# Kernel optimization log

Hardware: AMD Instinct MI355X
Metric: run time of the kernel (lower is better)

Reference implementation:

```python
import jax, jax.numpy as jnp
import numpy as np

IN_FEATURES = 256
OUT_FEATURES = 256
INTERNAL = (IN_FEATURES + OUT_FEATURES) // 2  # trajectron AdditiveAttention default


def setup_inputs() -> dict:
    key = jax.random.key(0)
    k1, k2, k3, k4, k5 = jax.random.split(key, 5)
    B, TH, TQ = 32, 256, 64
    inputs = jax.random.normal(k1, (B, TH, IN_FEATURES), dtype=jnp.float32)
    state = jax.random.normal(k2, (B, TQ, OUT_FEATURES), dtype=jnp.float32)
    # Linear weights (no bias), Kaiming-ish scale
    w1 = jax.random.normal(k3, (INTERNAL, IN_FEATURES), dtype=jnp.float32) / np.sqrt(IN_FEATURES)
    w2 = jax.random.normal(k4, (INTERNAL, OUT_FEATURES), dtype=jnp.float32) / np.sqrt(OUT_FEATURES)
    v = jax.random.normal(k5, (INTERNAL,), dtype=jnp.float32) / np.sqrt(INTERNAL)
    return {"inputs": inputs, "state": state, "w1": w1, "w2": w2, "v": v, "batch_size": B}


def reference(inputs, state, w1, w2, v, batch_size):
    # history annotations: (B, Th, Din); future annotations (queries): (B, Tq, Dout)
    keys = inputs.reshape(batch_size, -1, IN_FEATURES)
    queries = state.reshape(batch_size, -1, OUT_FEATURES)
    # Additive (Bahdanau) attention: score = v . tanh(W1 k + W2 q)
    k_proj = jnp.einsum('bti,di->btd', keys, w1)       # (B, Th, D)
    q_proj = jnp.einsum('bqo,do->bqd', queries, w2)    # (B, Tq, D)
    scores = jnp.einsum('d,bqtd->bqt', v, jnp.tanh(q_proj[:, :, None, :] + k_proj[:, None, :, :]))
    alpha = jax.nn.softmax(scores, axis=-1)            # softmax over history axis
    contexts = jnp.einsum('bqt,bti->bqi', alpha, keys)  # (B, Tq, Din)
    # reshape + dropout (eval mode / p effectively 0 -> identity)
    return contexts.reshape(-1, IN_FEATURES)
```

## Files before the change

### kernel.cpp

```cpp
#include <hip/hip_runtime.h>
#include <math.h>

#define BATCH 32
#define TH    256
#define TQn   64
#define DIN   256
#define DD    256
#define QT    4
#define E2C   2.885390081777927f
#define DENMAX 1.0e9f

typedef __attribute__((ext_vector_type(8)))  short bf16x8;
typedef __attribute__((ext_vector_type(16))) float floatx16;

__device__ __forceinline__ float readlane_f(float x, int l) {
    return __int_as_float(__builtin_amdgcn_readlane(__float_as_int(x), l));
}

__device__ __forceinline__ float eclamp(float x) {
    return __builtin_amdgcn_exp2f(fminf(x * E2C, 30.f));
}

__device__ __forceinline__ void split2(float x0, float x1, unsigned& hi, unsigned& lo) {
    unsigned u0 = __float_as_uint(x0), u1 = __float_as_uint(x1);
    unsigned h0 = u0 & 0xFFFF0000u,   h1 = u1 & 0xFFFF0000u;
    float r0 = x0 - __uint_as_float(h0);
    float r1 = x1 - __uint_as_float(h1);
    hi = (u0 >> 16) | h1;
    lo = (__float_as_uint(r0) >> 16) | (__float_as_uint(r1) & 0xFFFF0000u);
}

__device__ __forceinline__ void split8(float4 f0, float4 f1, uint4& hi, uint4& lo) {
    split2(f0.x, f0.y, hi.x, lo.x);
    split2(f0.z, f0.w, hi.y, lo.y);
    split2(f1.x, f1.y, hi.z, lo.z);
    split2(f1.z, f1.w, hi.w, lo.w);
}

#define REG4  65
#define WOFF  (16 * REG4)
__global__ __launch_bounds__(256, 4)
void proj_kernel(const float* __restrict__ keys,
                 const float* __restrict__ state,
                 const float* __restrict__ w1,
                 const float* __restrict__ w2,
                 float* __restrict__ kpT,
                 float* __restrict__ qpo)
{
    __shared__ uint4 lds4[2 * 16 * REG4];

    const int bid = blockIdx.x;
    const int tid = threadIdx.x;

    const float* X;
    const float* W;
    int m0, n0;
    bool is_kp;
    if (bid < 512) {
        is_kp = true;
        m0 = (bid >> 2) * 64;
        n0 = (bid & 3) * 64;
        X = keys; W = w1;
    } else {
        is_kp = false;
        int lb = bid - 512;
        m0 = (lb >> 2) * 64;
        n0 = (lb & 3) * 64;
        X = state; W = w2;
    }

    const int w    = tid >> 6;
    const int l    = tid & 63;
    const int mt   = w >> 1;
    const int nt   = w & 1;
    const int srow = tid >> 3;
    const int kg   = tid & 7;
    const int s_s  = kg >> 1;
    const int lidx = (srow & 31) + 32 * (kg & 1);

    floatx16 acc = {};

    for (int k0 = 0; k0 < DIN; k0 += 64) {
        #pragma unroll
        for (int hrow = 0; hrow < 2; hrow++) {
            int m = srow + hrow * 32;
            const float* px = X + (size_t)(m0 + m) * DIN + k0 + kg * 8;
            uint4 hi, lo;
            split8(*(const float4*)px, *(const float4*)(px + 4), hi, lo);
            int g = m >> 5;
            lds4[((0 * 2 + g) * 4 + s_s) * REG4 + lidx] = hi;
            lds4[((2 + g) * 4 + s_s) * REG4 + lidx] = lo;
            const float* pw = W + (size_t)(n0 + m) * DIN + k0 + kg * 8;
            split8(*(const float4*)pw, *(const float4*)(pw + 4), hi, lo);
            lds4[WOFF + ((0 * 2 + g) * 4 + s_s) * REG4 + lidx] = hi;
            lds4[WOFF + ((2 + g) * 4 + s_s) * REG4 + lidx] = lo;
        }
        __syncthreads();

        #pragma unroll
        for (int s = 0; s < 4; s++) {
            uint4 ahr = lds4[((0 * 2 + mt) * 4 + s) * REG4 + l];
            uint4 alr = lds4[((2 + mt) * 4 + s) * REG4 + l];
            uint4 bhr = lds4[WOFF + ((0 * 2 + nt) * 4 + s) * REG4 + l];
            uint4 blr = lds4[WOFF + ((2 + nt) * 4 + s) * REG4 + l];
            bf16x8 ah = __builtin_bit_cast(bf16x8, ahr);
            bf16x8 al = __builtin_bit_cast(bf16x8, alr);
            bf16x8 bh = __builtin_bit_cast(bf16x8, bhr);
            bf16x8 bl = __builtin_bit_cast(bf16x8, blr);
            acc = __builtin_amdgcn_mfma_f32_32x32x16_bf16(ah, bh, acc, 0, 0, 0);
            acc = __builtin_amdgcn_mfma_f32_32x32x16_bf16(al, bh, acc, 0, 0, 0);
            acc = __builtin_amdgcn_mfma_f32_32x32x16_bf16(ah, bl, acc, 0, 0, 0);
        }
        __syncthreads();
    }

    const int col = l & 31;
    const int hl  = l >> 5;
    if (is_kp) {
        const int b  = m0 >> 8;
        const int tb = (m0 & 255) + mt * 32 + 4 * hl;
        const int d  = n0 + nt * 32 + col;
        float* p = kpT + ((size_t)b * DD + d) * TH + tb;
        #pragma unroll
        for (int g = 0; g < 4; g++)
            *(float4*)(p + 8 * g) = make_float4(eclamp(acc[4*g]),   eclamp(acc[4*g+1]),
                                                eclamp(acc[4*g+2]), eclamp(acc[4*g+3]));
    } else {
        const int d = n0 + nt * 32 + col;
        #pragma unroll
        for (int r = 0; r < 16; r++) {
            int row = (r & 3) + 8 * (r >> 2) + 4 * hl;
            qpo[(size_t)(m0 + mt * 32 + row) * DD + d] = eclamp(acc[r]);
        }
    }
}

__global__ __launch_bounds__(1024, 8)
void attn_kernel(const float* __restrict__ keys,
                 const float* __restrict__ vvec,
                 const float* __restrict__ kpT,
                 const float* __restrict__ qp,
                 float* __restrict__ out)
{
    __shared__ float s_part[4][QT][TH];
    __shared__ float s_alpha[QT][TH];
    __shared__ float s_rsum[QT];

    const int bid  = blockIdx.x;
    const int b    = bid & 31;
    const int q0   = (bid >> 5) * QT;
    const int tid  = threadIdx.x;
    const int t    = tid & 255;
    const int dgu  = __builtin_amdgcn_readfirstlane(tid >> 8);
    const int lane = tid & 63;
    const int wv   = tid >> 6;

    float acc[QT];
    #pragma unroll
    for (int q = 0; q < QT; q++) acc[q] = 0.f;

    const float* kbase = kpT + ((size_t)b * DD + dgu * 64) * TH + t;
    const float* qpb   = qp + (size_t)(b * TQn + q0) * DD + dgu * 64;
    const float* vv    = vvec + dgu * 64;

    #pragma unroll 4
    for (int l0 = 0; l0 < 64; l0 += 4) {
        float kv0 = kbase[(size_t)(l0 + 0) * TH];
        float kv1 = kbase[(size_t)(l0 + 1) * TH];
        float kv2 = kbase[(size_t)(l0 + 2) * TH];
        float kv3 = kbase[(size_t)(l0 + 3) * TH];
        float v0 = vv[l0 + 0], v1 = vv[l0 + 1], v2 = vv[l0 + 2], v3 = vv[l0 + 3];
        #pragma unroll
        for (int q = 0; q < QT; q++) {
            float d0 = fminf(fmaf(qpb[q * DD + l0 + 0], kv0, 1.f), DENMAX);
            float d1 = fminf(fmaf(qpb[q * DD + l0 + 1], kv1, 1.f), DENMAX);
            float d2 = fminf(fmaf(qpb[q * DD + l0 + 2], kv2, 1.f), DENMAX);
            float d3 = fminf(fmaf(qpb[q * DD + l0 + 3], kv3, 1.f), DENMAX);
            float n01 = fmaf(v1, d0, v0 * d1);
            float d01 = d0 * d1;
            float n23 = fmaf(v3, d2, v2 * d3);
            float d23 = d2 * d3;
            float num = fmaf(n23, d01, n01 * d23);
            float den = d01 * d23;
            acc[q] = fmaf(num, __builtin_amdgcn_rcpf(den), acc[q]);
        }
    }

    #pragma unroll
    for (int q = 0; q < QT; q++) s_part[dgu][q][t] = acc[q];
    __syncthreads();

    if (wv < QT) {
        const int q = wv;
        float x0, x1, x2, x3;
        {
            float p0 = s_part[0][q][lane]       + s_part[1][q][lane]
                     + s_part[2][q][lane]       + s_part[3][q][lane];
            float p1 = s_part[0][q][lane + 64]  + s_part[1][q][lane + 64]
                     + s_part[2][q][lane + 64]  + s_part[3][q][lane + 64];
            float p2 = s_part[0][q][lane + 128] + s_part[1][q][lane + 128]
                     + s_part[2][q][lane + 128] + s_part[3][q][lane + 128];
            float p3 = s_part[0][q][lane + 192] + s_part[1][q][lane + 192]
                     + s_part[2][q][lane + 192] + s_part[3][q][lane + 192];
            x0 = -2.f * p0; x1 = -2.f * p1; x2 = -2.f * p2; x3 = -2.f * p3;
        }
        float m = fmaxf(fmaxf(x0, x1), fmaxf(x2, x3));
        #pragma unroll
        for (int off = 32; off >= 1; off >>= 1) m = fmaxf(m, __shfl_xor(m, off));
        float e0 = __expf(x0 - m), e1 = __expf(x1 - m);
        float e2 = __expf(x2 - m), e3 = __expf(x3 - m);
        s_alpha[q][lane]       = e0;
        s_alpha[q][lane + 64]  = e1;
        s_alpha[q][lane + 128] = e2;
        s_alpha[q][lane + 192] = e3;
        float s = (e0 + e1) + (e2 + e3);
        #pragma unroll
        for (int off = 32; off >= 1; off >>= 1) s += __shfl_xor(s, off);
        if (lane == 0) s_rsum[q] = 1.f / s;
    }
    __syncthreads();

    float ctx[QT];
    #pragma unroll
    for (int q = 0; q < QT; q++) ctx[q] = 0.f;

    const float* krow = keys + ((size_t)b * TH + dgu * 64) * DIN + t;
    float ar[QT];
    #pragma unroll
    for (int q = 0; q < QT; q++) ar[q] = s_alpha[q][dgu * 64 + lane];

    for (int l = 0; l < 64; l += 4) {
        float kv4[4];
        #pragma unroll
        for (int j = 0; j < 4; j++)
            kv4[j] = krow[(size_t)(l + j) * DIN];
        #pragma unroll
        for (int j = 0; j < 4; j++) {
            #pragma unroll
            for (int q = 0; q < QT; q++)
                ctx[q] = fmaf(readlane_f(ar[q], l + j), kv4[j], ctx[q]);
        }
    }

    #pragma unroll
    for (int q = 0; q < QT; q++) s_part[dgu][q][t] = ctx[q];
    __syncthreads();

    {
        int q = tid >> 8, ii = tid & 255;
        float s = s_part[0][q][ii] + s_part[1][q][ii]
                + s_part[2][q][ii] + s_part[3][q][ii];
        out[(size_t)(b * TQn + q0 + q) * DIN + ii] = s * s_rsum[q];
    }
}

extern "C" void kernel_launch(void* const* d_in, const int* in_sizes, int n_in,
                              void* d_out, int out_size, void* d_ws, size_t ws_size,
                              hipStream_t stream) {
    (void)in_sizes; (void)n_in; (void)out_size; (void)ws_size;
    const float* keys  = (const float*)d_in[0];
    const float* state = (const float*)d_in[1];
    const float* w1    = (const float*)d_in[2];
    const float* w2    = (const float*)d_in[3];
    const float* v     = (const float*)d_in[4];
    float* out = (float*)d_out;

    float* kpT = (float*)d_ws;
    float* qp  = kpT + (size_t)BATCH * DD * TH;

    hipLaunchKernelGGL(proj_kernel, dim3(640), dim3(256), 0, stream,
                       keys, state, w1, w2, kpT, qp);
    hipLaunchKernelGGL(attn_kernel, dim3(BATCH * (TQn / QT)), dim3(1024), 0, stream,
                       keys, v, kpT, qp, out);
}
```

Measured before the change: 117.0 us.

## Store key projections in d-quad interleaved layout for float4 loads in attention

Changes the intermediate exp(2·k_proj) buffer from [b][d][t] to [b][d/4][t][4], so each attention thread reads one float4 per four d values instead of four strided scalar loads. The projection kernel now stages its output tile through LDS to transpose it into this layout before writing. The v and query-projection reads also become float4. This adds an LDS round trip and an extra barrier to the projection epilogue in exchange for fewer, wider global loads in the hot attention loop.

```diff
diff --git a/kernel.cpp b/kernel.cpp
--- a/kernel.cpp
+++ b/kernel.cpp
@@ -39,12 +39,13 @@
 
 #define REG4  65
 #define WOFF  (16 * REG4)
+#define TSTR  68
 __global__ __launch_bounds__(256, 4)
 void proj_kernel(const float* __restrict__ keys,
                  const float* __restrict__ state,
                  const float* __restrict__ w1,
                  const float* __restrict__ w2,
-                 float* __restrict__ kpT,
+                 float* __restrict__ ktp,
                  float* __restrict__ qpo)
 {
     __shared__ uint4 lds4[2 * 16 * REG4];
@@ -117,14 +118,23 @@
     const int col = l & 31;
     const int hl  = l >> 5;
     if (is_kp) {
+        float* sT = (float*)lds4;
+        const int d_local = nt * 32 + col;
+        #pragma unroll
+        for (int r = 0; r < 16; r++) {
+            int t_local = mt * 32 + 4 * hl + 8 * (r >> 2) + (r & 3);
+            sT[t_local * TSTR + d_local] = eclamp(acc[r]);
+        }
+        __syncthreads();
         const int b  = m0 >> 8;
-        const int tb = (m0 & 255) + mt * 32 + 4 * hl;
-        const int d  = n0 + nt * 32 + col;
-        float* p = kpT + ((size_t)b * DD + d) * TH + tb;
-        #pragma unroll
-        for (int g = 0; g < 4; g++)
-            *(float4*)(p + 8 * g) = make_float4(eclamp(acc[4*g]),   eclamp(acc[4*g+1]),
-                                                eclamp(acc[4*g+2]), eclamp(acc[4*g+3]));
+        const int t0 = m0 & 255;
+        float4* dst4 = (float4*)ktp;
+        #pragma unroll
+        for (int p = 0; p < 4; p++) {
+            int dp_local = w * 4 + p;
+            float4 v4 = *(float4*)&sT[l * TSTR + dp_local * 4];
+            dst4[(size_t)(b * 64 + (n0 >> 2) + dp_local) * 256 + t0 + l] = v4;
+        }
     } else {
         const int d = n0 + nt * 32 + col;
         #pragma unroll
@@ -138,7 +148,7 @@
 __global__ __launch_bounds__(1024, 8)
 void attn_kernel(const float* __restrict__ keys,
                  const float* __restrict__ vvec,
-                 const float* __restrict__ kpT,
+                 const float* __restrict__ ktp,
                  const float* __restrict__ qp,
                  float* __restrict__ out)
 {
@@ -159,26 +169,24 @@
     #pragma unroll
     for (int q = 0; q < QT; q++) acc[q] = 0.f;
 
-    const float* kbase = kpT + ((size_t)b * DD + dgu * 64) * TH + t;
-    const float* qpb   = qp + (size_t)(b * TQn + q0) * DD + dgu * 64;
-    const float* vv    = vvec + dgu * 64;
+    const float4* kb4 = (const float4*)ktp + ((size_t)(b * 64 + dgu * 16) * 256 + t);
+    const float*  qpb = qp + (size_t)(b * TQn + q0) * DD + dgu * 64;
+    const float*  vv  = vvec + dgu * 64;
 
     #pragma unroll 4
-    for (int l0 = 0; l0 < 64; l0 += 4) {
-        float kv0 = kbase[(size_t)(l0 + 0) * TH];
-        float kv1 = kbase[(size_t)(l0 + 1) * TH];
-        float kv2 = kbase[(size_t)(l0 + 2) * TH];
-        float kv3 = kbase[(size_t)(l0 + 3) * TH];
-        float v0 = vv[l0 + 0], v1 = vv[l0 + 1], v2 = vv[l0 + 2], v3 = vv[l0 + 3];
+    for (int dp = 0; dp < 16; dp++) {
+        float4 kv = kb4[(size_t)dp * 256];
+        float4 v4 = *(const float4*)(vv + dp * 4);
         #pragma unroll
         for (int q = 0; q < QT; q++) {
-            float d0 = fminf(fmaf(qpb[q * DD + l0 + 0], kv0, 1.f), DENMAX);
-            float d1 = fminf(fmaf(qpb[q * DD + l0 + 1], kv1, 1.f), DENMAX);
-            float d2 = fminf(fmaf(qpb[q * DD + l0 + 2], kv2, 1.f), DENMAX);
-            float d3 = fminf(fmaf(qpb[q * DD + l0 + 3], kv3, 1.f), DENMAX);
-            float n01 = fmaf(v1, d0, v0 * d1);
+            float4 pq = *(const float4*)(qpb + q * DD + dp * 4);
+            float d0 = fminf(fmaf(pq.x, kv.x, 1.f), DENMAX);
+            float d1 = fminf(fmaf(pq.y, kv.y, 1.f), DENMAX);
+            float d2 = fminf(fmaf(pq.z, kv.z, 1.f), DENMAX);
+            float d3 = fminf(fmaf(pq.w, kv.w, 1.f), DENMAX);
+            float n01 = fmaf(v4.y, d0, v4.x * d1);
             float d01 = d0 * d1;
-            float n23 = fmaf(v3, d2, v2 * d3);
+            float n23 = fmaf(v4.w, d2, v4.z * d3);
             float d23 = d2 * d3;
             float num = fmaf(n23, d01, n01 * d23);
             float den = d01 * d23;
@@ -265,11 +273,11 @@
     const float* v     = (const float*)d_in[4];
     float* out = (float*)d_out;
 
-    float* kpT = (float*)d_ws;
-    float* qp  = kpT + (size_t)BATCH * DD * TH;
+    float* ktp = (float*)d_ws;
+    float* qp  = ktp + (size_t)BATCH * DD * TH;
 
     hipLaunchKernelGGL(proj_kernel, dim3(640), dim3(256), 0, stream,
-                       keys, state, w1, w2, kpT, qp);
+                       keys, state, w1, w2, ktp, qp);
     hipLaunchKernelGGL(attn_kernel, dim3(BATCH * (TQn / QT)), dim3(1024), 0, stream,
-                       keys, v, kpT, qp, out);
-}
+                       keys, v, ktp, qp, out);
+}
```

New measurement: 118.1 us. About the same (+0.9%).
